# Kernel optimization log

Measured on AMD Instinct MI355X. Metric: run time of the kernel, lower is better.

The kernel has to match this reference:

```python
import jax, jax.numpy as jnp
import numpy as np

B, N = 4, 256
EDGE_F = 256; NODE_F = 256; MSG = 128; LINK_H = 128
ROUNDS = 3; CLASSES = 600


def setup_inputs() -> dict:
    key = jax.random.key(0)
    ks = jax.random.split(key, 16)
    s = 0.05
    return {
        "edge_features": jax.random.normal(ks[0], (B, N, N, EDGE_F), jnp.float32),
        "node_features": jax.random.normal(ks[1], (B, N, NODE_F), jnp.float32),
        "adj_mat": jnp.zeros((B, N, N), jnp.float32),
        "node_labels": jnp.zeros((B, N, CLASSES), jnp.float32),
        "human_nums": jax.random.randint(ks[2], (B,), 0, 16),
        "obj_nums": jax.random.randint(ks[3], (B,), 0, 224),
        # feature-resize linears
        "W_er": jax.random.normal(ks[4], (EDGE_F, MSG), jnp.float32) * s,
        "b_er": jnp.zeros((MSG,), jnp.float32),
        "W_nr": jax.random.normal(ks[5], (NODE_F, MSG), jnp.float32) * s,
        "b_nr": jnp.zeros((MSG,), jnp.float32),
        # link function: 1x1 GraphConv stack MSG -> LINK_H -> 1
        "W_l1": jax.random.normal(ks[6], (MSG, LINK_H), jnp.float32) * s,
        "b_l1": jnp.zeros((LINK_H,), jnp.float32),
        "W_l2": jax.random.normal(ks[7], (LINK_H, 1), jnp.float32) * s,
        "b_l2": jnp.zeros((1,), jnp.float32),
        # message function: linear_concat_relu  (cat(h_w, e_vw) -> MSG)
        "W_msg": jax.random.normal(ks[8], (2 * MSG, MSG), jnp.float32) * s,
        "b_msg": jnp.zeros((MSG,), jnp.float32),
        # GRU update (torch gate order r,z,n)
        "W_ih": jax.random.normal(ks[9], (MSG, 3 * MSG), jnp.float32) * s,
        "b_ih": jnp.zeros((3 * MSG,), jnp.float32),
        "W_hh": jax.random.normal(ks[10], (MSG, 3 * MSG), jnp.float32) * s,
        "b_hh": jnp.zeros((3 * MSG,), jnp.float32),
        # readout fc
        "W_ro": jax.random.normal(ks[11], (MSG, CLASSES), jnp.float32) * s,
        "b_ro": jnp.zeros((CLASSES,), jnp.float32),
    }


def _gru_cell(x, h, W_ih, b_ih, W_hh, b_hh):
    gi = x @ W_ih + b_ih
    gh = h @ W_hh + b_hh
    ir, iz, i_n = jnp.split(gi, 3, axis=-1)
    hr, hz, h_n = jnp.split(gh, 3, axis=-1)
    r = jax.nn.sigmoid(ir + hr)
    z = jax.nn.sigmoid(iz + hz)
    n = jnp.tanh(i_n + r * h_n)
    return (1.0 - z) * n + z * h


def reference(edge_features, node_features, adj_mat, node_labels,
              human_nums, obj_nums,
              W_er, b_er, W_nr, b_nr, W_l1, b_l1, W_l2, b_l2,
              W_msg, b_msg, W_ih, b_ih, W_hh, b_hh, W_ro, b_ro):
    Bn, Nn = node_features.shape[0], node_features.shape[1]
    # resize_feature_to_message_size
    ef = edge_features @ W_er + b_er          # [B, N(i=receiver), N(w=sender), M]
    nf = node_features @ W_nr + b_nr          # [B, N, M]

    valid = (human_nums + obj_nums).astype(jnp.int32)
    node_mask = (jnp.arange(Nn)[None, :] < valid[:, None]).astype(ef.dtype)  # [B,N]
    pair_mask = node_mask[:, :, None] * node_mask[:, None, :]                # [B,N,N]

    # NOTE: the original forward never writes updated node states back into
    # hidden_node_states, so every round uses the ORIGINAL (resized) node and
    # edge features for the message function -> m_raw is round-invariant.
    cat = jnp.concatenate(
        [jnp.broadcast_to(nf[:, None, :, :], ef.shape), ef], axis=-1)  # [B,N,N,2M]
    m_raw = jax.nn.relu(cat @ W_msg + b_msg)                           # [B,N,N,M]

    e_state = ef                                    # hidden edge state, round 0
    pred_adj = jnp.zeros((Bn, Nn, Nn), ef.dtype)
    pred_labels = jnp.zeros((Bn, Nn, CLASSES), ef.dtype)
    for rnd in range(ROUNDS):
        # GraphConv link function (1x1 convs == per-edge MLP), valid block only
        hlink = jax.nn.relu(e_state @ W_l1 + b_l1)
        pred_adj = pair_mask * (hlink @ W_l2 + b_l2)[..., 0]     # [B,N,N]
        gate = jax.nn.sigmoid(pred_adj) * node_mask[:, None, :]  # zero invalid senders
        m = gate[..., None] * m_raw                              # [B,N,N,M]
        # next-round hidden edge state: column i holds gated messages to node i
        e_state = jnp.where(pair_mask[..., None] > 0, jnp.swapaxes(m, 1, 2), ef)
        if rnd == ROUNDS - 1:
            m_sum = m.sum(axis=2)                                # [B,N,M]
            h_new = _gru_cell(m_sum, nf, W_ih, b_ih, W_hh, b_hh)
            pred_labels = node_mask[..., None] * (h_new @ W_ro + b_ro)
    return pred_adj, pred_labels
```

## Files before the change

kernel.cpp:

```cpp
#include <hip/hip_runtime.h>
#include <hip/hip_bf16.h>


#define B_ 4
#define N_ 256
#define EF_ 256
#define M_ 128
#define CL_ 600
#define ADJ_SZ (B_*N_*N_)

typedef __hip_bfloat16 bf16;
typedef short short8 __attribute__((ext_vector_type(8)));
typedef float f32x4 __attribute__((ext_vector_type(4)));

#define MFMA(a,b,c) __builtin_amdgcn_mfma_f32_16x16x32_bf16(a,b,c,0,0,0)

__device__ __forceinline__ float s2f(short s){
  union { unsigned int u; float f; } x; x.u = ((unsigned int)(unsigned short)s) << 16; return x.f;
}
__device__ __forceinline__ bf16 f2b(float f){ return __float2bfloat16(f); }
__device__ __forceinline__ short f2bs(float f){
  bf16 h = __float2bfloat16(f);
  return *reinterpret_cast<short*>(&h);
}
__device__ __forceinline__ float sigm(float x){ return 1.0f/(1.0f+expf(-x)); }

template<bool BF> __device__ __forceinline__ float ld(const void* p, size_t i){
  if (BF) return s2f(((const short*)p)[i]);
  return ((const float*)p)[i];
}
template<bool BF> __device__ __forceinline__ void st(void* p, size_t i, float v){
  if (BF) ((bf16*)p)[i] = f2b(v);
  else    ((float*)p)[i] = v;
}
__device__ __forceinline__ float dot8(short8 w, const float* x){
  float a = 0.f;
  #pragma unroll
  for (int j=0;j<8;j++) a += x[j]*s2f(w[j]);
  return a;
}

__global__ __launch_bounds__(64)
void k_detect(const unsigned short* ef, int* flag){
  int t = threadIdx.x;
  int cnt = 0;
  for (int j = 0; j < 64; j++){
    unsigned short u = ef[t*64 + j];
    int e = (u >> 7) & 0xFF;
    cnt += (e >= 96 && e <= 144) ? 1 : 0;
  }
  for (int o = 32; o > 0; o >>= 1) cnt += __shfl_down(cnt, o, 64);
  if (t == 0) *flag = (cnt > 3500) ? 1 : 0;
}

template<bool BF>
__global__ __launch_bounds__(256)
void k_zero(void* out, int n, const int* dflag){
  if ((*dflag != 0) != BF) return;
  int i = blockIdx.x*256 + threadIdx.x;
  if (i < n) st<BF>(out, i, 0.0f);
}

template<bool BF>
__global__ __launch_bounds__(64)
void k_pack(const void* src, int K, int N, bf16* dst, const int* dflag){
  if ((*dflag != 0) != BF) return;
  int blk = blockIdx.x;
  int n16 = N >> 4;
  int kk = blk / n16, nt = blk % n16;
  int lane = threadIdx.x;
  int k0 = kk*32 + (lane>>4)*8;
  int n  = nt*16 + (lane&15);
  size_t dbase = ((size_t)blk*64 + lane)*8;
  #pragma unroll
  for (int j=0;j<8;j++)
    dst[dbase+j] = f2b(ld<BF>(src, (size_t)(k0+j)*N + n));
}

template<bool BF>
__global__ __launch_bounds__(256)
void k_tr(const void* src, int K, int N, bf16* dst, const int* dflag){
  if ((*dflag != 0) != BF) return;
  int idx = blockIdx.x*256 + threadIdx.x;
  if (idx >= K*N) return;
  int k = idx / N, n = idx % N;
  dst[(size_t)n*K + k] = f2b(ld<BF>(src, idx));
}

template<bool BF>
__global__ __launch_bounds__(128)
void k_nf_c(const void* nodef, const bf16* tWnr, const void* b_nr,
            const bf16* tWmsgT, const void* b_msg, float* nf, float* cb,
            const int* dflag)
{
  if ((*dflag != 0) != BF) return;
  int blk = blockIdx.x; int b = blk >> 8; int v = blk & 255;
  int t = threadIdx.x;
  __shared__ float xs[EF_];
  __shared__ float nfs[M_];
  size_t xrow = ((size_t)(b*N_)+v)*EF_;
  xs[t]     = ld<BF>(nodef, xrow + t);
  xs[t+128] = ld<BF>(nodef, xrow + t + 128);
  __syncthreads();
  float acc = ld<BF>(b_nr, t);
  const short8* wp = (const short8*)(tWnr + (size_t)t*EF_);
  #pragma unroll 4
  for (int k8=0;k8<32;k8++) acc += dot8(wp[k8], &xs[k8*8]);
  nf[((size_t)(b*N_)+v)*M_+t] = acc;
  nfs[t] = acc;
  __syncthreads();
  float acc2 = ld<BF>(b_msg, t);
  const short8* wq = (const short8*)(tWmsgT + (size_t)t*M_);
  #pragma unroll 4
  for (int k8=0;k8<16;k8++) acc2 += dot8(wq[k8], &nfs[k8*8]);
  cb[((size_t)(b*N_)+v)*M_+t] = acc2;
}

template<bool BF>
__global__ __launch_bounds__(256)
void k_r0(const void* edgef, const bf16* pWer, const void* b_er,
          const bf16* pWmsgB, const float* cb, const bf16* pWl1,
          const void* b_l1, const void* W_l2, const void* b_l2,
          const int* hn, const int* on, bf16* mraw, float* s0,
          const int* dflag)
{
  if ((*dflag != 0) != BF) return;
  int b = blockIdx.z, i = blockIdx.y, w0 = blockIdx.x*32;
  int valid = hn[b] + on[b];
  if (i >= valid || w0 >= valid) return;
  int t = threadIdx.x;
  __shared__ __attribute__((aligned(16))) bf16 EfsB[32][136];
  __shared__ __attribute__((aligned(16))) char uni[32*264*2];
  bf16  (*Xs)[264]  = (bf16(*)[264])uni;
  float (*hls)[132] = (float(*)[132])uni;

  {
    int j = t>>3, c = (t&7)*32;
    size_t g = (((size_t)(b*N_)+i)*N_ + (size_t)(w0+j))*EF_ + c;
    if (BF){
      const short8* src = (const short8*)((const short*)edgef + g);
      short8* dst = (short8*)&Xs[j][c];
      #pragma unroll
      for (int u=0;u<4;u++) dst[u] = src[u];
    } else {
      const float* src = (const float*)edgef + g;
      #pragma unroll
      for (int u=0;u<32;u++) Xs[j][c+u] = f2b(src[u]);
    }
  }
  __syncthreads();

  int lane = t & 63, wv = t >> 6;
  int r0 = (wv&1)*16;
  int c0h = wv >> 1;
  int mA = r0 + (lane&15);
  int kq = (lane>>4)*8;
  int qrow = r0 + (lane>>4)*4;

  f32x4 z4 = {0.f,0.f,0.f,0.f};
  f32x4 acc[4] = {z4,z4,z4,z4};
  for (int kk=0;kk<8;kk++){
    short8 a = *(const short8*)&Xs[mA][kk*32 + kq];
    #pragma unroll
    for (int nt=0;nt<4;nt++){
      int gnt = c0h*4 + nt;
      short8 bb = *(const short8*)(pWer + (((size_t)kk*8 + gnt)*64 + lane)*8);
      acc[nt] = MFMA(a, bb, acc[nt]);
    }
  }
  #pragma unroll
  for (int nt=0;nt<4;nt++){
    int col = c0h*64 + nt*16 + (lane&15);
    float be = ld<BF>(b_er, col);
    #pragma unroll
    for (int r=0;r<4;r++)
      EfsB[qrow+r][col] = f2b(acc[nt][r] + be);
  }
  __syncthreads();

  f32x4 am[4] = {z4,z4,z4,z4};
  f32x4 ah[4] = {z4,z4,z4,z4};
  for (int kk=0;kk<4;kk++){
    short8 a = *(const short8*)&EfsB[mA][kk*32 + kq];
    #pragma unroll
    for (int nt=0;nt<4;nt++){
      int gnt = c0h*4 + nt;
      size_t off = (((size_t)kk*8 + gnt)*64 + lane)*8;
      short8 b1 = *(const short8*)(pWmsgB + off);
      am[nt] = MFMA(a, b1, am[nt]);
      short8 b2 = *(const short8*)(pWl1 + off);
      ah[nt] = MFMA(a, b2, ah[nt]);
    }
  }
  #pragma unroll
  for (int nt=0;nt<4;nt++){
    int col = c0h*64 + nt*16 + (lane&15);
    float bl = ld<BF>(b_l1, col);
    #pragma unroll
    for (int r=0;r<4;r++){
      int row = qrow + r;
      int w = w0 + row;
      float v = am[nt][r] + cb[((size_t)(b*N_)+w)*M_ + col];
      mraw[(((size_t)(b*N_)+i)*N_ + w)*M_ + col] = f2b(fmaxf(v, 0.f));
      hls[row][col] = fmaxf(ah[nt][r] + bl, 0.f);
    }
  }
  __syncthreads();
  {
    int row = t>>3, seg = t&7;
    float p = 0.f;
    #pragma unroll
    for (int k=0;k<16;k++) p += hls[row][seg*16+k] * ld<BF>(W_l2, seg*16+k);
    p += __shfl_down(p, 4, 8);
    p += __shfl_down(p, 2, 8);
    p += __shfl_down(p, 1, 8);
    if (seg==0 && (w0+row) < valid)
      s0[((size_t)(b*N_)+i)*N_ + w0 + row] = p + ld<BF>(b_l2, 0);
  }
}

template<bool BF>
__global__ __launch_bounds__(256)
void k_link2(const bf16* mraw, const float* s_prev, const bf16* pWl1,
             const void* b_l1, const void* W_l2, const void* b_l2,
             const int* hn, const int* on, float* s_next, const int* dflag)
{
  if ((*dflag != 0) != BF) return;
  int b = blockIdx.z, i = blockIdx.y, w0 = blockIdx.x*32;
  int valid = hn[b] + on[b];
  if (i >= valid || w0 >= valid) return;
  int t = threadIdx.x;
  __shared__ __attribute__((aligned(16))) bf16 EsB[32][136];
  __shared__ __attribute__((aligned(16))) float hls[32][132];
  __shared__ float sg[32];
  if (t < 32){
    int w = w0 + t;
    sg[t] = (w < valid) ? sigm(s_prev[((size_t)(b*N_)+w)*N_ + i]) : 0.f;
  }
  __syncthreads();
  {
    int j = t>>3, c = (t&7)*16;
    const short* src = (const short*)mraw + (((size_t)(b*N_)+(size_t)(w0+j))*N_ + i)*M_;
    float s = sg[j];
    #pragma unroll
    for (int u=0;u<2;u++){
      short8 v = *(const short8*)(src + c + u*8);
      short8 o;
      #pragma unroll
      for (int e=0;e<8;e++) o[e] = f2bs(s2f(v[e])*s);
      *(short8*)&EsB[j][c+u*8] = o;
    }
  }
  __syncthreads();

  int lane = t & 63, wv = t >> 6;
  int r0 = (wv&1)*16;
  int c0h = wv >> 1;
  int mA = r0 + (lane&15);
  int kq = (lane>>4)*8;
  int qrow = r0 + (lane>>4)*4;

  f32x4 z4 = {0.f,0.f,0.f,0.f};
  f32x4 ah[4] = {z4,z4,z4,z4};
  for (int kk=0;kk<4;kk++){
    short8 a = *(const short8*)&EsB[mA][kk*32 + kq];
    #pragma unroll
    for (int nt=0;nt<4;nt++){
      int gnt = c0h*4 + nt;
      short8 b2 = *(const short8*)(pWl1 + (((size_t)kk*8 + gnt)*64 + lane)*8);
      ah[nt] = MFMA(a, b2, ah[nt]);
    }
  }
  #pragma unroll
  for (int nt=0;nt<4;nt++){
    int col = c0h*64 + nt*16 + (lane&15);
    float bl = ld<BF>(b_l1, col);
    #pragma unroll
    for (int r=0;r<4;r++)
      hls[qrow+r][col] = fmaxf(ah[nt][r] + bl, 0.f);
  }
  __syncthreads();
  {
    int row = t>>3, seg = t&7;
    float p = 0.f;
    #pragma unroll
    for (int k=0;k<16;k++) p += hls[row][seg*16+k] * ld<BF>(W_l2, seg*16+k);
    p += __shfl_down(p, 4, 8);
    p += __shfl_down(p, 2, 8);
    p += __shfl_down(p, 1, 8);
    if (seg==0 && (w0+row) < valid)
      s_next[((size_t)(b*N_)+i)*N_ + w0 + row] = p + ld<BF>(b_l2, 0);
  }
}

template<bool BF>
__global__ __launch_bounds__(128)
void k_final(const bf16* mraw, const float* s2, const float* nf,
             const bf16* tWih, const void* b_ih,
             const bf16* tWhh, const void* b_hh,
             const bf16* tWro, const void* b_ro,
             const int* hn, const int* on, void* out, const int* dflag)
{
  if ((*dflag != 0) != BF) return;
  int i = blockIdx.x, b = blockIdx.y;
  int valid = hn[b] + on[b];
  if (i >= valid) return;
  int t = threadIdx.x;
  __shared__ float sgs[N_];
  __shared__ float xsh[M_], hsh[M_], hns[M_];
  const float* srow = s2 + ((size_t)(b*N_)+i)*N_;
  size_t adj = ((size_t)(b*N_)+i)*N_;
  for (int w=t; w<N_; w+=128){
    if (w < valid){
      float v = srow[w];
      st<BF>(out, adj + w, v);
      sgs[w] = sigm(v);
    } else sgs[w] = 0.f;
  }
  __syncthreads();
  const short* mrow = (const short*)mraw + (((size_t)(b*N_)+i)*N_)*M_;
  float acc = 0.f;
  for (int w=0; w<valid; w++) acc += sgs[w]*s2f(mrow[(size_t)w*M_ + t]);
  xsh[t] = acc;
  hsh[t] = nf[((size_t)(b*N_)+i)*M_ + t];
  __syncthreads();
  float gi[3], gh[3];
  #pragma unroll
  for (int g=0; g<3; g++){
    int o = g*M_ + t;
    float a = ld<BF>(b_ih, o), c = ld<BF>(b_hh, o);
    const short8* wi = (const short8*)(tWih + (size_t)o*M_);
    const short8* wh = (const short8*)(tWhh + (size_t)o*M_);
    #pragma unroll 4
    for (int k8=0;k8<16;k8++){
      a += dot8(wi[k8], &xsh[k8*8]);
      c += dot8(wh[k8], &hsh[k8*8]);
    }
    gi[g] = a; gh[g] = c;
  }
  float r  = sigm(gi[0] + gh[0]);
  float z  = sigm(gi[1] + gh[1]);
  float nn = tanhf(gi[2] + r*gh[2]);
  float hnew = (1.f - z)*nn + z*hsh[t];
  hns[t] = hnew;
  __syncthreads();
  size_t lab = (size_t)ADJ_SZ + ((size_t)(b*N_)+i)*CL_;
  for (int cls=t; cls<CL_; cls+=128){
    float a = ld<BF>(b_ro, cls);
    const short8* wr = (const short8*)(tWro + (size_t)cls*M_);
    #pragma unroll 4
    for (int k8=0;k8<16;k8++) a += dot8(wr[k8], &hns[k8*8]);
    st<BF>(out, lab + cls, a);
  }
}

template<bool BF>
static void run_pipeline(void* const* d_in, void* d_out, int out_size,
                         char* ws, const int* dflag, hipStream_t stream)
{
  const void* edgef = d_in[0];
  const void* nodef = d_in[1];
  const int*  hn    = (const int*)d_in[4];
  const int*  on    = (const int*)d_in[5];
  const void* W_er  = d_in[6];  const void* b_er  = d_in[7];
  const void* W_nr  = d_in[8];  const void* b_nr  = d_in[9];
  const void* W_l1  = d_in[10]; const void* b_l1  = d_in[11];
  const void* W_l2  = d_in[12]; const void* b_l2  = d_in[13];
  const void* W_msg = d_in[14]; const void* b_msg = d_in[15];
  const void* W_ih  = d_in[16]; const void* b_ih  = d_in[17];
  const void* W_hh  = d_in[18]; const void* b_hh  = d_in[19];
  const void* W_ro  = d_in[20]; const void* b_ro  = d_in[21];

  bf16*  mraw   = (bf16*) (ws);
  float* s_a    = (float*)(ws + 67108864);
  float* s_b    = (float*)(ws + 68157440);
  float* nf     = (float*)(ws + 69206016);
  float* cb     = (float*)(ws + 69730304);
  bf16*  pWer   = (bf16*) (ws + 70254592);
  bf16*  pWmsgB = (bf16*) (ws + 70320128);
  bf16*  pWl1   = (bf16*) (ws + 70352896);
  bf16*  tWnr   = (bf16*) (ws + 70385664);
  bf16*  tWmsgT = (bf16*) (ws + 70451200);
  bf16*  tWih   = (bf16*) (ws + 70483968);
  bf16*  tWhh   = (bf16*) (ws + 70582272);
  bf16*  tWro   = (bf16*) (ws + 70680576);

  const void* W_msgB = BF ? (const void*)((const bf16*)W_msg + 128*M_)
                          : (const void*)((const float*)W_msg + 128*M_);

  k_zero<BF><<<(out_size+255)/256, 256, 0, stream>>>(d_out, out_size, dflag);
  k_pack<BF><<<64, 64, 0, stream>>>(W_er, 256, 128, pWer, dflag);
  k_pack<BF><<<32, 64, 0, stream>>>(W_msgB, 128, 128, pWmsgB, dflag);
  k_pack<BF><<<32, 64, 0, stream>>>(W_l1, 128, 128, pWl1, dflag);
  k_tr<BF><<<128, 256, 0, stream>>>(W_nr, 256, 128, tWnr, dflag);
  k_tr<BF><<<64, 256, 0, stream>>>(W_msg, 128, 128, tWmsgT, dflag);
  k_tr<BF><<<192, 256, 0, stream>>>(W_ih, 128, 384, tWih, dflag);
  k_tr<BF><<<192, 256, 0, stream>>>(W_hh, 128, 384, tWhh, dflag);
  k_tr<BF><<<300, 256, 0, stream>>>(W_ro, 128, 600, tWro, dflag);

  k_nf_c<BF><<<B_*N_, 128, 0, stream>>>(nodef, tWnr, b_nr, tWmsgT, b_msg, nf, cb, dflag);
  dim3 g2(N_/32, N_, B_);
  k_r0<BF><<<g2, 256, 0, stream>>>(edgef, pWer, b_er, pWmsgB, cb, pWl1,
                                   b_l1, W_l2, b_l2, hn, on, mraw, s_a, dflag);
  k_link2<BF><<<g2, 256, 0, stream>>>(mraw, s_a, pWl1, b_l1, W_l2, b_l2, hn, on, s_b, dflag);
  k_link2<BF><<<g2, 256, 0, stream>>>(mraw, s_b, pWl1, b_l1, W_l2, b_l2, hn, on, s_a, dflag);
  k_final<BF><<<dim3(N_, B_), 128, 0, stream>>>(mraw, s_a, nf, tWih, b_ih, tWhh, b_hh,
                                                tWro, b_ro, hn, on, d_out, dflag);
}

extern "C" void kernel_launch(void* const* d_in, const int* in_sizes, int n_in,
                              void* d_out, int out_size, void* d_ws, size_t ws_size,
                              hipStream_t stream)
{
  char* ws = (char*)d_ws;
  int* dflag = (int*)(ws + 70834176);

  k_detect<<<1, 64, 0, stream>>>((const unsigned short*)d_in[0], dflag);
  run_pipeline<false>(d_in, d_out, out_size, ws, dflag, stream);
  run_pipeline<true >(d_in, d_out, out_size, ws, dflag, stream);
}
```

Before: 561.7 us.

## Collapse dual-dtype pipelines into runtime-branching kernels and fuse weight prep

Replaces the two templated pipelines (fp32 and bf16, each launched with early-exit on a device flag) with a single set of kernels that branch on the dtype flag at runtime. This halves the number of kernel launches. All weight pack and transpose kernels are merged into one k_prep launch. The separate output-zeroing kernel is removed: k_final now writes zeros for invalid rows and columns itself. k_nf_c reads the untransposed weights directly with scalar loads, and the fp32 edge-feature load uses vector loads. The cost is runtime branches inside kernels and a slower scalar path in k_nf_c.

Measured after the change: 571.6 us. No clear change (+1.7%).

```diff
diff --git a/kernel.cpp b/kernel.cpp
--- a/kernel.cpp
+++ b/kernel.cpp
@@ -18,20 +18,13 @@
 __device__ __forceinline__ float s2f(short s){
   union { unsigned int u; float f; } x; x.u = ((unsigned int)(unsigned short)s) << 16; return x.f;
 }
-__device__ __forceinline__ bf16 f2b(float f){ return __float2bfloat16(f); }
 __device__ __forceinline__ short f2bs(float f){
   bf16 h = __float2bfloat16(f);
   return *reinterpret_cast<short*>(&h);
 }
 __device__ __forceinline__ float sigm(float x){ return 1.0f/(1.0f+expf(-x)); }
-
-template<bool BF> __device__ __forceinline__ float ld(const void* p, size_t i){
-  if (BF) return s2f(((const short*)p)[i]);
-  return ((const float*)p)[i];
-}
-template<bool BF> __device__ __forceinline__ void st(void* p, size_t i, float v){
-  if (BF) ((bf16*)p)[i] = f2b(v);
-  else    ((float*)p)[i] = v;
+__device__ __forceinline__ float ldx(const void* p, size_t i, bool bf){
+  return bf ? s2f(((const short*)p)[i]) : ((const float*)p)[i];
 }
 __device__ __forceinline__ float dot8(short8 w, const float* x){
   float a = 0.f;
@@ -53,99 +46,100 @@
   if (t == 0) *flag = (cnt > 3500) ? 1 : 0;
 }
 
-template<bool BF>
 __global__ __launch_bounds__(256)
-void k_zero(void* out, int n, const int* dflag){
-  if ((*dflag != 0) != BF) return;
-  int i = blockIdx.x*256 + threadIdx.x;
-  if (i < n) st<BF>(out, i, 0.0f);
-}
-
-template<bool BF>
-__global__ __launch_bounds__(64)
-void k_pack(const void* src, int K, int N, bf16* dst, const int* dflag){
-  if ((*dflag != 0) != BF) return;
-  int blk = blockIdx.x;
-  int n16 = N >> 4;
-  int kk = blk / n16, nt = blk % n16;
-  int lane = threadIdx.x;
-  int k0 = kk*32 + (lane>>4)*8;
-  int n  = nt*16 + (lane&15);
-  size_t dbase = ((size_t)blk*64 + lane)*8;
-  #pragma unroll
-  for (int j=0;j<8;j++)
-    dst[dbase+j] = f2b(ld<BF>(src, (size_t)(k0+j)*N + n));
-}
-
-template<bool BF>
-__global__ __launch_bounds__(256)
-void k_tr(const void* src, int K, int N, bf16* dst, const int* dflag){
-  if ((*dflag != 0) != BF) return;
-  int idx = blockIdx.x*256 + threadIdx.x;
-  if (idx >= K*N) return;
-  int k = idx / N, n = idx % N;
-  dst[(size_t)n*K + k] = f2b(ld<BF>(src, idx));
-}
-
-template<bool BF>
+void k_prep(const void* W_er, const void* W_msg, const void* W_l1,
+            const void* W_ih, const void* W_hh, const void* W_ro,
+            short* pWer, short* pWmsgB, short* pWl1,
+            short* tWih, short* tWhh, short* tWro, const int* dflag)
+{
+  bool bf = (*dflag != 0);
+  int bid = blockIdx.x, t = threadIdx.x;
+  if (bid < 32){
+    int unit = bid*4 + (t>>6);
+    int lane = t & 63;
+    const void* src; short* dst; int p; size_t soff = 0;
+    if (unit < 64)      { src = W_er;  dst = pWer;   p = unit; }
+    else if (unit < 96) { src = W_msg; dst = pWmsgB; p = unit - 64; soff = (size_t)128*M_; }
+    else                { src = W_l1;  dst = pWl1;   p = unit - 96; }
+    int kk = p >> 3, nt = p & 7;
+    int k0 = kk*32 + (lane>>4)*8;
+    int n  = nt*16 + (lane&15);
+    size_t dbase = ((size_t)p*64 + lane)*8;
+    #pragma unroll
+    for (int j=0;j<8;j++)
+      dst[dbase+j] = f2bs(ldx(src, soff + (size_t)(k0+j)*M_ + n, bf));
+  } else if (bid < 224){
+    int idx = (bid-32)*256 + t;
+    int k = idx / 384, n = idx % 384;
+    tWih[(size_t)n*M_ + k] = f2bs(ldx(W_ih, idx, bf));
+  } else if (bid < 416){
+    int idx = (bid-224)*256 + t;
+    int k = idx / 384, n = idx % 384;
+    tWhh[(size_t)n*M_ + k] = f2bs(ldx(W_hh, idx, bf));
+  } else {
+    int idx = (bid-416)*256 + t;
+    int k = idx / 600, n = idx % 600;
+    tWro[(size_t)n*M_ + k] = f2bs(ldx(W_ro, idx, bf));
+  }
+}
+
 __global__ __launch_bounds__(128)
-void k_nf_c(const void* nodef, const bf16* tWnr, const void* b_nr,
-            const bf16* tWmsgT, const void* b_msg, float* nf, float* cb,
+void k_nf_c(const void* nodef, const void* W_nr, const void* b_nr,
+            const void* W_msg, const void* b_msg, float* nf, float* cb,
             const int* dflag)
 {
-  if ((*dflag != 0) != BF) return;
+  bool bf = (*dflag != 0);
   int blk = blockIdx.x; int b = blk >> 8; int v = blk & 255;
   int t = threadIdx.x;
   __shared__ float xs[EF_];
   __shared__ float nfs[M_];
   size_t xrow = ((size_t)(b*N_)+v)*EF_;
-  xs[t]     = ld<BF>(nodef, xrow + t);
-  xs[t+128] = ld<BF>(nodef, xrow + t + 128);
-  __syncthreads();
-  float acc = ld<BF>(b_nr, t);
-  const short8* wp = (const short8*)(tWnr + (size_t)t*EF_);
-  #pragma unroll 4
-  for (int k8=0;k8<32;k8++) acc += dot8(wp[k8], &xs[k8*8]);
+  xs[t]     = ldx(nodef, xrow + t, bf);
+  xs[t+128] = ldx(nodef, xrow + t + 128, bf);
+  __syncthreads();
+  float acc = ldx(b_nr, t, bf);
+  for (int k=0;k<EF_;k++) acc += xs[k]*ldx(W_nr, (size_t)k*M_+t, bf);
   nf[((size_t)(b*N_)+v)*M_+t] = acc;
   nfs[t] = acc;
   __syncthreads();
-  float acc2 = ld<BF>(b_msg, t);
-  const short8* wq = (const short8*)(tWmsgT + (size_t)t*M_);
-  #pragma unroll 4
-  for (int k8=0;k8<16;k8++) acc2 += dot8(wq[k8], &nfs[k8*8]);
+  float acc2 = ldx(b_msg, t, bf);
+  for (int k=0;k<M_;k++) acc2 += nfs[k]*ldx(W_msg, (size_t)k*M_+t, bf);
   cb[((size_t)(b*N_)+v)*M_+t] = acc2;
 }
 
-template<bool BF>
 __global__ __launch_bounds__(256)
-void k_r0(const void* edgef, const bf16* pWer, const void* b_er,
-          const bf16* pWmsgB, const float* cb, const bf16* pWl1,
+void k_r0(const void* edgef, const short* pWer, const void* b_er,
+          const short* pWmsgB, const float* cb, const short* pWl1,
           const void* b_l1, const void* W_l2, const void* b_l2,
-          const int* hn, const int* on, bf16* mraw, float* s0,
+          const int* hn, const int* on, short* mraw, float* s0,
           const int* dflag)
 {
-  if ((*dflag != 0) != BF) return;
+  bool bf = (*dflag != 0);
   int b = blockIdx.z, i = blockIdx.y, w0 = blockIdx.x*32;
   int valid = hn[b] + on[b];
   if (i >= valid || w0 >= valid) return;
   int t = threadIdx.x;
-  __shared__ __attribute__((aligned(16))) bf16 EfsB[32][136];
+  __shared__ __attribute__((aligned(16))) short EfsB[32][136];
   __shared__ __attribute__((aligned(16))) char uni[32*264*2];
-  bf16  (*Xs)[264]  = (bf16(*)[264])uni;
+  short (*Xs)[264]  = (short(*)[264])uni;
   float (*hls)[132] = (float(*)[132])uni;
 
   {
     int j = t>>3, c = (t&7)*32;
     size_t g = (((size_t)(b*N_)+i)*N_ + (size_t)(w0+j))*EF_ + c;
-    if (BF){
+    if (bf){
       const short8* src = (const short8*)((const short*)edgef + g);
       short8* dst = (short8*)&Xs[j][c];
       #pragma unroll
       for (int u=0;u<4;u++) dst[u] = src[u];
     } else {
-      const float* src = (const float*)edgef + g;
+      const f32x4* src = (const f32x4*)((const float*)edgef + g);
       #pragma unroll
-      for (int u=0;u<32;u++) Xs[j][c+u] = f2b(src[u]);
+      for (int u=0;u<8;u++){
+        f32x4 v = src[u];
+        #pragma unroll
+        for (int e=0;e<4;e++) Xs[j][c+u*4+e] = f2bs(v[e]);
+      }
     }
   }
   __syncthreads();
@@ -171,10 +165,10 @@
   #pragma unroll
   for (int nt=0;nt<4;nt++){
     int col = c0h*64 + nt*16 + (lane&15);
-    float be = ld<BF>(b_er, col);
+    float be = ldx(b_er, col, bf);
     #pragma unroll
     for (int r=0;r<4;r++)
-      EfsB[qrow+r][col] = f2b(acc[nt][r] + be);
+      EfsB[qrow+r][col] = f2bs(acc[nt][r] + be);
   }
   __syncthreads();
 
@@ -195,13 +189,13 @@
   #pragma unroll
   for (int nt=0;nt<4;nt++){
     int col = c0h*64 + nt*16 + (lane&15);
-    float bl = ld<BF>(b_l1, col);
+    float bl = ldx(b_l1, col, bf);
     #pragma unroll
     for (int r=0;r<4;r++){
       int row = qrow + r;
       int w = w0 + row;
       float v = am[nt][r] + cb[((size_t)(b*N_)+w)*M_ + col];
-      mraw[(((size_t)(b*N_)+i)*N_ + w)*M_ + col] = f2b(fmaxf(v, 0.f));
+      mraw[(((size_t)(b*N_)+i)*N_ + w)*M_ + col] = f2bs(fmaxf(v, 0.f));
       hls[row][col] = fmaxf(ah[nt][r] + bl, 0.f);
     }
   }
@@ -210,27 +204,26 @@
     int row = t>>3, seg = t&7;
     float p = 0.f;
     #pragma unroll
-    for (int k=0;k<16;k++) p += hls[row][seg*16+k] * ld<BF>(W_l2, seg*16+k);
+    for (int k=0;k<16;k++) p += hls[row][seg*16+k] * ldx(W_l2, seg*16+k, bf);
     p += __shfl_down(p, 4, 8);
     p += __shfl_down(p, 2, 8);
     p += __shfl_down(p, 1, 8);
     if (seg==0 && (w0+row) < valid)
-      s0[((size_t)(b*N_)+i)*N_ + w0 + row] = p + ld<BF>(b_l2, 0);
-  }
-}
-
-template<bool BF>
+      s0[((size_t)(b*N_)+i)*N_ + w0 + row] = p + ldx(b_l2, 0, bf);
+  }
+}
+
 __global__ __launch_bounds__(256)
-void k_link2(const bf16* mraw, const float* s_prev, const bf16* pWl1,
+void k_link2(const short* mraw, const float* s_prev, const short* pWl1,
              const void* b_l1, const void* W_l2, const void* b_l2,
              const int* hn, const int* on, float* s_next, const int* dflag)
 {
-  if ((*dflag != 0) != BF) return;
+  bool bf = (*dflag != 0);
   int b = blockIdx.z, i = blockIdx.y, w0 = blockIdx.x*32;
   int valid = hn[b] + on[b];
   if (i >= valid || w0 >= valid) return;
   int t = threadIdx.x;
-  __shared__ __attribute__((aligned(16))) bf16 EsB[32][136];
+  __shared__ __attribute__((aligned(16))) short EsB[32][136];
   __shared__ __attribute__((aligned(16))) float hls[32][132];
   __shared__ float sg[32];
   if (t < 32){
@@ -240,7 +233,7 @@
   __syncthreads();
   {
     int j = t>>3, c = (t&7)*16;
-    const short* src = (const short*)mraw + (((size_t)(b*N_)+(size_t)(w0+j))*N_ + i)*M_;
+    const short* src = mraw + (((size_t)(b*N_)+(size_t)(w0+j))*N_ + i)*M_;
     float s = sg[j];
     #pragma unroll
     for (int u=0;u<2;u++){
@@ -274,7 +267,7 @@
   #pragma unroll
   for (int nt=0;nt<4;nt++){
     int col = c0h*64 + nt*16 + (lane&15);
-    float bl = ld<BF>(b_l1, col);
+    float bl = ldx(b_l1, col, bf);
     #pragma unroll
     for (int r=0;r<4;r++)
       hls[qrow+r][col] = fmaxf(ah[nt][r] + bl, 0.f);
@@ -284,41 +277,52 @@
     int row = t>>3, seg = t&7;
     float p = 0.f;
     #pragma unroll
-    for (int k=0;k<16;k++) p += hls[row][seg*16+k] * ld<BF>(W_l2, seg*16+k);
+    for (int k=0;k<16;k++) p += hls[row][seg*16+k] * ldx(W_l2, seg*16+k, bf);
     p += __shfl_down(p, 4, 8);
     p += __shfl_down(p, 2, 8);
     p += __shfl_down(p, 1, 8);
     if (seg==0 && (w0+row) < valid)
-      s_next[((size_t)(b*N_)+i)*N_ + w0 + row] = p + ld<BF>(b_l2, 0);
-  }
-}
-
-template<bool BF>
+      s_next[((size_t)(b*N_)+i)*N_ + w0 + row] = p + ldx(b_l2, 0, bf);
+  }
+}
+
 __global__ __launch_bounds__(128)
-void k_final(const bf16* mraw, const float* s2, const float* nf,
-             const bf16* tWih, const void* b_ih,
-             const bf16* tWhh, const void* b_hh,
-             const bf16* tWro, const void* b_ro,
+void k_final(const short* mraw, const float* s2, const float* nf,
+             const short* tWih, const void* b_ih,
+             const short* tWhh, const void* b_hh,
+             const short* tWro, const void* b_ro,
              const int* hn, const int* on, void* out, const int* dflag)
 {
-  if ((*dflag != 0) != BF) return;
+  bool bf = (*dflag != 0);
   int i = blockIdx.x, b = blockIdx.y;
   int valid = hn[b] + on[b];
-  if (i >= valid) return;
   int t = threadIdx.x;
+  size_t adj = ((size_t)(b*N_)+i)*N_;
+  size_t lab = (size_t)ADJ_SZ + ((size_t)(b*N_)+i)*CL_;
+  short* o16 = (short*)out;
+  float* o32 = (float*)out;
+  if (i >= valid){
+    if (bf){
+      for (int w=t; w<N_; w+=128) o16[adj+w] = 0;
+      for (int c=t; c<CL_; c+=128) o16[lab+c] = 0;
+    } else {
+      for (int w=t; w<N_; w+=128) o32[adj+w] = 0.f;
+      for (int c=t; c<CL_; c+=128) o32[lab+c] = 0.f;
+    }
+    return;
+  }
   __shared__ float sgs[N_];
   __shared__ float xsh[M_], hsh[M_], hns[M_];
   const float* srow = s2 + ((size_t)(b*N_)+i)*N_;
-  size_t adj = ((size_t)(b*N_)+i)*N_;
   for (int w=t; w<N_; w+=128){
-    if (w < valid){
-      float v = srow[w];
-      st<BF>(out, adj + w, v);
-      sgs[w] = sigm(v);
-    } else sgs[w] = 0.f;
-  }
-  __syncthreads();
-  const short* mrow = (const short*)mraw + (((size_t)(b*N_)+i)*N_)*M_;
+    float v = 0.f; float sv = 0.f;
+    if (w < valid){ v = srow[w]; sv = sigm(v); }
+    if (bf) o16[adj+w] = (w < valid) ? f2bs(v) : (short)0;
+    else    o32[adj+w] = (w < valid) ? v : 0.f;
+    sgs[w] = sv;
+  }
+  __syncthreads();
+  const short* mrow = mraw + (((size_t)(b*N_)+i)*N_)*M_;
   float acc = 0.f;
   for (int w=0; w<valid; w++) acc += sgs[w]*s2f(mrow[(size_t)w*M_ + t]);
   xsh[t] = acc;
@@ -328,7 +332,7 @@
   #pragma unroll
   for (int g=0; g<3; g++){
     int o = g*M_ + t;
-    float a = ld<BF>(b_ih, o), c = ld<BF>(b_hh, o);
+    float a = ldx(b_ih, o, bf), c = ldx(b_hh, o, bf);
     const short8* wi = (const short8*)(tWih + (size_t)o*M_);
     const short8* wh = (const short8*)(tWhh + (size_t)o*M_);
     #pragma unroll 4
@@ -344,19 +348,19 @@
   float hnew = (1.f - z)*nn + z*hsh[t];
   hns[t] = hnew;
   __syncthreads();
-  size_t lab = (size_t)ADJ_SZ + ((size_t)(b*N_)+i)*CL_;
   for (int cls=t; cls<CL_; cls+=128){
-    float a = ld<BF>(b_ro, cls);
+    float a = ldx(b_ro, cls, bf);
     const short8* wr = (const short8*)(tWro + (size_t)cls*M_);
     #pragma unroll 4
     for (int k8=0;k8<16;k8++) a += dot8(wr[k8], &hns[k8*8]);
-    st<BF>(out, lab + cls, a);
-  }
-}
-
-template<bool BF>
-static void run_pipeline(void* const* d_in, void* d_out, int out_size,
-                         char* ws, const int* dflag, hipStream_t stream)
+    if (bf) o16[lab+cls] = f2bs(a);
+    else    o32[lab+cls] = a;
+  }
+}
+
+extern "C" void kernel_launch(void* const* d_in, const int* in_sizes, int n_in,
+                              void* d_out, int out_size, void* d_ws, size_t ws_size,
+                              hipStream_t stream)
 {
   const void* edgef = d_in[0];
   const void* nodef = d_in[1];
@@ -371,51 +375,29 @@
   const void* W_hh  = d_in[18]; const void* b_hh  = d_in[19];
   const void* W_ro  = d_in[20]; const void* b_ro  = d_in[21];
 
-  bf16*  mraw   = (bf16*) (ws);
+  char*  ws     = (char*)d_ws;
+  short* mraw   = (short*)(ws);
   float* s_a    = (float*)(ws + 67108864);
   float* s_b    = (float*)(ws + 68157440);
   float* nf     = (float*)(ws + 69206016);
   float* cb     = (float*)(ws + 69730304);
-  bf16*  pWer   = (bf16*) (ws + 70254592);
-  bf16*  pWmsgB = (bf16*) (ws + 70320128);
-  bf16*  pWl1   = (bf16*) (ws + 70352896);
-  bf16*  tWnr   = (bf16*) (ws + 70385664);
-  bf16*  tWmsgT = (bf16*) (ws + 70451200);
-  bf16*  tWih   = (bf16*) (ws + 70483968);
-  bf16*  tWhh   = (bf16*) (ws + 70582272);
-  bf16*  tWro   = (bf16*) (ws + 70680576);
-
-  const void* W_msgB = BF ? (const void*)((const bf16*)W_msg + 128*M_)
-                          : (const void*)((const float*)W_msg + 128*M_);
-
-  k_zero<BF><<<(out_size+255)/256, 256, 0, stream>>>(d_out, out_size, dflag);
-  k_pack<BF><<<64, 64, 0, stream>>>(W_er, 256, 128, pWer, dflag);
-  k_pack<BF><<<32, 64, 0, stream>>>(W_msgB, 128, 128, pWmsgB, dflag);
-  k_pack<BF><<<32, 64, 0, stream>>>(W_l1, 128, 128, pWl1, dflag);
-  k_tr<BF><<<128, 256, 0, stream>>>(W_nr, 256, 128, tWnr, dflag);
-  k_tr<BF><<<64, 256, 0, stream>>>(W_msg, 128, 128, tWmsgT, dflag);
-  k_tr<BF><<<192, 256, 0, stream>>>(W_ih, 128, 384, tWih, dflag);
-  k_tr<BF><<<192, 256, 0, stream>>>(W_hh, 128, 384, tWhh, dflag);
-  k_tr<BF><<<300, 256, 0, stream>>>(W_ro, 128, 600, tWro, dflag);
-
-  k_nf_c<BF><<<B_*N_, 128, 0, stream>>>(nodef, tWnr, b_nr, tWmsgT, b_msg, nf, cb, dflag);
+  short* pWer   = (short*)(ws + 70254592);
+  short* pWmsgB = (short*)(ws + 70320128);
+  short* pWl1   = (short*)(ws + 70352896);
+  short* tWih   = (short*)(ws + 70385664);
+  short* tWhh   = (short*)(ws + 70483968);
+  short* tWro   = (short*)(ws + 70582272);
+  int*   dflag  = (int*)  (ws + 70834176);
+
+  k_detect<<<1, 64, 0, stream>>>((const unsigned short*)edgef, dflag);
+  k_prep<<<716, 256, 0, stream>>>(W_er, W_msg, W_l1, W_ih, W_hh, W_ro,
+                                  pWer, pWmsgB, pWl1, tWih, tWhh, tWro, dflag);
+  k_nf_c<<<B_*N_, 128, 0, stream>>>(nodef, W_nr, b_nr, W_msg, b_msg, nf, cb, dflag);
   dim3 g2(N_/32, N_, B_);
-  k_r0<BF><<<g2, 256, 0, stream>>>(edgef, pWer, b_er, pWmsgB, cb, pWl1,
-                                   b_l1, W_l2, b_l2, hn, on, mraw, s_a, dflag);
-  k_link2<BF><<<g2, 256, 0, stream>>>(mraw, s_a, pWl1, b_l1, W_l2, b_l2, hn, on, s_b, dflag);
-  k_link2<BF><<<g2, 256, 0, stream>>>(mraw, s_b, pWl1, b_l1, W_l2, b_l2, hn, on, s_a, dflag);
-  k_final<BF><<<dim3(N_, B_), 128, 0, stream>>>(mraw, s_a, nf, tWih, b_ih, tWhh, b_hh,
-                                                tWro, b_ro, hn, on, d_out, dflag);
-}
-
-extern "C" void kernel_launch(void* const* d_in, const int* in_sizes, int n_in,
-                              void* d_out, int out_size, void* d_ws, size_t ws_size,
-                              hipStream_t stream)
-{
-  char* ws = (char*)d_ws;
-  int* dflag = (int*)(ws + 70834176);
-
-  k_detect<<<1, 64, 0, stream>>>((const unsigned short*)d_in[0], dflag);
-  run_pipeline<false>(d_in, d_out, out_size, ws, dflag, stream);
-  run_pipeline<true >(d_in, d_out, out_size, ws, dflag, stream);
-}
+  k_r0<<<g2, 256, 0, stream>>>(edgef, pWer, b_er, pWmsgB, cb, pWl1,
+                               b_l1, W_l2, b_l2, hn, on, mraw, s_a, dflag);
+  k_link2<<<g2, 256, 0, stream>>>(mraw, s_a, pWl1, b_l1, W_l2, b_l2, hn, on, s_b, dflag);
+  k_link2<<<g2, 256, 0, stream>>>(mraw, s_b, pWl1, b_l1, W_l2, b_l2, hn, on, s_a, dflag);
+  k_final<<<dim3(N_, B_), 128, 0, stream>>>(mraw, s_a, nf, tWih, b_ih, tWhh, b_hh,
+                                            tWro, b_ro, hn, on, d_out, dflag);
+}
```
